# Kernel optimization log

Hardware: AMD Instinct MI355X
Metric: run time of the kernel (lower is better)

Reference implementation:

```python
import jax, jax.numpy as jnp
import numpy as np

N_NODES = 50000
N_EDGES = 800000
IN_CH = 128
OUT_CH = 64
HEADS = 4
NEG_SLOPE = 0.2  # PyG GATConv default


def setup_inputs() -> dict:
    key = jax.random.key(0)
    k1, k2, k3, k4, k5 = jax.random.split(key, 5)
    x = jax.random.normal(k1, (N_NODES, IN_CH), dtype=jnp.float32)
    edge_index = jax.random.randint(k2, (2, N_EDGES), 0, N_NODES, dtype=jnp.int64)
    W = jax.random.normal(k3, (HEADS * OUT_CH, IN_CH), dtype=jnp.float32) * (1.0 / np.sqrt(IN_CH))
    att_src = jax.random.normal(k4, (HEADS, OUT_CH), dtype=jnp.float32) * (1.0 / np.sqrt(OUT_CH))
    att_dst = jax.random.normal(k5, (HEADS, OUT_CH), dtype=jnp.float32) * (1.0 / np.sqrt(OUT_CH))
    bias = jnp.zeros((OUT_CH,), dtype=jnp.float32)
    return {"x": x, "edge_index": edge_index, "W": W,
            "att_src": att_src, "att_dst": att_dst, "bias": bias}


def reference(x, edge_index, W, att_src, att_dst, bias):
    # GAT2NO_NORM.forward in eval mode: dropout == identity.
    N = x.shape[0]
    H, C = att_src.shape
    # PyG GATConv adds self-loops by default.
    loop = jnp.arange(N, dtype=edge_index.dtype)
    src = jnp.concatenate([edge_index[0], loop])  # message source j
    dst = jnp.concatenate([edge_index[1], loop])  # message target i
    # Linear projection, reshape to heads: [N, H, C]
    h = (x @ W.T).reshape(N, H, C)
    # Per-node attention halves: [N, H]
    a_src = jnp.einsum('nhc,hc->nh', h, att_src)
    a_dst = jnp.einsum('nhc,hc->nh', h, att_dst)
    # Per-edge raw score, LeakyReLU: [E, H]
    e = jax.nn.leaky_relu(a_src[src] + a_dst[dst], NEG_SLOPE)
    # Segment (edge-)softmax over incoming edges of each dst node.
    m = jax.lax.stop_gradient(jax.ops.segment_max(e, dst, num_segments=N))
    ex = jnp.exp(e - m[dst])
    denom = jax.ops.segment_sum(ex, dst, num_segments=N)
    alpha = ex / denom[dst]  # self-loops guarantee denom > 0
    # Weighted scatter-sum of messages: [N, H, C]
    msg = h[src] * alpha[:, :, None]
    out = jax.ops.segment_sum(msg, dst, num_segments=N)
    # concat=False -> mean over heads, then bias, then ReLU (module wrapper)
    out = out.mean(axis=1) + bias
    return jax.nn.relu(out)
```

## Files before the change

kernel.cpp:

```cpp
#include <hip/hip_runtime.h>
#include <hip/hip_fp16.h>
#include <math.h>

#define N_NODES 50000
#define N_EDGES 800000
#define IN_CH 128
#define PROJ_CH 256
#define OUT_CH 64
#define HEADS 4
#define NEG_SLOPE 0.2f
#define CAP 80
#define PROJ_BLOCKS 782
#define GRID_BLOCKS 3125

typedef _Float16 f16x8 __attribute__((ext_vector_type(8)));
typedef _Float16 f16x4 __attribute__((ext_vector_type(4)));
typedef __fp16   hf2   __attribute__((ext_vector_type(2)));
typedef float    f32x4 __attribute__((ext_vector_type(4)));

__device__ __forceinline__ float leaky(float v) {
    return v > 0.f ? v : NEG_SLOPE * v;
}

__device__ __forceinline__ hf2 u32_as_h2(unsigned int u) {
    union { unsigned int u; hf2 h; } c; c.u = u; return c.h;
}

__global__ __launch_bounds__(256) void prep_kernel(
    const float* __restrict__ W, _Float16* __restrict__ Wh, int* __restrict__ cnt)
{
    const int t = blockIdx.x * 256 + threadIdx.x;
    if (t < PROJ_CH * IN_CH) Wh[t] = (_Float16)W[t];
    if (t < N_NODES) cnt[t] = 0;
}

__global__ __launch_bounds__(256) void mega_kernel(
    const float* __restrict__ x, const _Float16* __restrict__ Wh,
    const float* __restrict__ att_src, const float* __restrict__ att_dst,
    const int* __restrict__ ei, int* __restrict__ cnt, unsigned short* __restrict__ csr,
    _Float16* __restrict__ h, float* __restrict__ a_src, float* __restrict__ a_dst)
{
    __shared__ _Float16 xs[64 * 136];
    const int tid = threadIdx.x;
    const int bid = blockIdx.x;

    const int e = bid * 256 + tid;
    const int esrc = ei[e];
    const int edst = ei[N_EDGES + e];
    const int pos = atomicAdd(&cnt[edst], 1);

    if (bid >= PROJ_BLOCKS) {
        if (pos < CAP) csr[edst * CAP + pos] = (unsigned short)esrc;
        return;
    }

    const int w    = tid >> 6;
    const int lane = tid & 63;
    const int q    = lane >> 4;
    const int l15  = lane & 15;
    const int nb   = bid * 64;

    float4 xv[8];
#pragma unroll
    for (int r = 0; r < 8; ++r) {
        int v   = r * 256 + tid;
        int row = v >> 5;
        int c4  = v & 31;
        int grow = nb + row;
        if (grow > N_NODES - 1) grow = N_NODES - 1;
        xv[r] = *(const float4*)(x + (size_t)grow * IN_CH + c4 * 4);
    }

    f16x8 B[4][4];
#pragma unroll
    for (int k0i = 0; k0i < 4; ++k0i)
#pragma unroll
        for (int n0i = 0; n0i < 4; ++n0i) {
            const int oc = w * 64 + n0i * 16 + l15;
            B[k0i][n0i] = *(const f16x8*)(Wh + (size_t)oc * IN_CH + k0i * 32 + q * 8);
        }

#pragma unroll
    for (int r = 0; r < 8; ++r) {
        int v   = r * 256 + tid;
        int row = v >> 5;
        int c4  = v & 31;
        f16x4 hv;
        hv[0] = (_Float16)xv[r].x; hv[1] = (_Float16)xv[r].y;
        hv[2] = (_Float16)xv[r].z; hv[3] = (_Float16)xv[r].w;
        *(f16x4*)&xs[row * 136 + c4 * 4] = hv;
    }
    __syncthreads();

    f32x4 acc[4][4];
#pragma unroll
    for (int m0i = 0; m0i < 4; ++m0i)
#pragma unroll
        for (int n0i = 0; n0i < 4; ++n0i)
            acc[m0i][n0i] = (f32x4){0.f, 0.f, 0.f, 0.f};

#pragma unroll
    for (int k0i = 0; k0i < 4; ++k0i) {
        f16x8 A[4];
#pragma unroll
        for (int m0i = 0; m0i < 4; ++m0i)
            A[m0i] = *(const f16x8*)&xs[(m0i * 16 + l15) * 136 + k0i * 32 + q * 8];
#pragma unroll
        for (int n0i = 0; n0i < 4; ++n0i)
#pragma unroll
            for (int m0i = 0; m0i < 4; ++m0i)
                acc[m0i][n0i] = __builtin_amdgcn_mfma_f32_16x16x32_f16(
                    A[m0i], B[k0i][n0i], acc[m0i][n0i], 0, 0, 0);
    }

    float att_s[4], att_d[4];
#pragma unroll
    for (int n0i = 0; n0i < 4; ++n0i) {
        att_s[n0i] = att_src[w * 64 + n0i * 16 + l15];
        att_d[n0i] = att_dst[w * 64 + n0i * 16 + l15];
    }

#pragma unroll
    for (int m0i = 0; m0i < 4; ++m0i) {
        float vs[4], vd[4];
#pragma unroll
        for (int r = 0; r < 4; ++r) {
            float s = 0.f, d = 0.f;
#pragma unroll
            for (int n0i = 0; n0i < 4; ++n0i) {
                s = fmaf(acc[m0i][n0i][r], att_s[n0i], s);
                d = fmaf(acc[m0i][n0i][r], att_d[n0i], d);
            }
            vs[r] = s; vd[r] = d;
        }
#pragma unroll
        for (int off = 1; off < 16; off <<= 1) {
#pragma unroll
            for (int r = 0; r < 4; ++r) {
                vs[r] += __shfl_xor(vs[r], off, 64);
                vd[r] += __shfl_xor(vd[r], off, 64);
            }
        }
#pragma unroll
        for (int r = 0; r < 4; ++r) {
            int node = nb + m0i * 16 + q * 4 + r;
            if (l15 == 0 && node < N_NODES) {
                a_src[node * HEADS + w] = vs[r];
                a_dst[node * HEADS + w] = vd[r];
            }
        }
    }

    unsigned char* lb = (unsigned char*)xs;
    __syncthreads();
#pragma unroll
    for (int p = 0; p < 2; ++p) {
#pragma unroll
        for (int mm = 0; mm < 2; ++mm) {
            const int m0i = 2 * p + mm;
            const int nl0 = mm * 16 + q * 4;
#pragma unroll
            for (int n0i = 0; n0i < 4; ++n0i) {
                const int ch = w * 64 + n0i * 16 + l15;
#pragma unroll
                for (int r = 0; r < 4; ++r)
                    *(_Float16*)(lb + (nl0 + r) * 528 + ch * 2) =
                        (_Float16)acc[m0i][n0i][r];
            }
        }
        __syncthreads();
#pragma unroll
        for (int r = 0; r < 4; ++r) {
            int idx  = r * 256 + tid;
            int nl   = idx >> 5;
            int ck   = idx & 31;
            int node = nb + p * 32 + nl;
            if (node < N_NODES) {
                f16x8 vv = *(const f16x8*)(lb + nl * 528 + ck * 16);
                *(f16x8*)(h + (size_t)node * PROJ_CH + ck * 8) = vv;
            }
        }
        if (p == 0) __syncthreads();
    }

    if (pos < CAP) csr[edst * CAP + pos] = (unsigned short)esrc;
}

__global__ __launch_bounds__(256) void aggregate_kernel(
    const _Float16* __restrict__ h, const float* __restrict__ a_src,
    const float* __restrict__ a_dst, const int* __restrict__ cnt,
    const unsigned short* __restrict__ csr, const float* __restrict__ bias,
    float* __restrict__ out)
{
    const int tid  = threadIdx.x;
    const int wave = tid >> 6;
    const int l    = tid & 63;
    const int i    = blockIdx.x * 4 + wave;

    __shared__ float lw_all[4][(CAP + 1) * 4];
    __shared__ int   lj_all[4][CAP + 4];
    float* lw = lw_all[wave];
    int*   lj = lj_all[wave];

    const int n    = min(cnt[i], CAP);
    const int base = i * CAP;
    const int h4   = l & 3;
    const float adh = a_dst[i * 4 + h4];

    float lsum = 0.f;
    {
        float ws = __expf(leaky(a_src[i * 4 + h4] + adh));
        if (l < 4) { lw[l] = ws; lsum = ws; }
        if (l == 0) lj[0] = i;
    }

    const int erel = l >> 2;
    for (int p0 = 0; p0 < n; p0 += 16) {
        int e = p0 + erel;
        bool valid = e < n;
        int j = valid ? (int)csr[base + e] : 0;
        float w = 0.f;
        if (valid) w = __expf(leaky(a_src[j * 4 + h4] + adh));
        lsum += w;
        lw[(e + 1) * 4 + h4] = w;
        if (h4 == 0) lj[e + 1] = j;
    }
#pragma unroll
    for (int off = 4; off < 64; off <<= 1) lsum += __shfl_xor(lsum, off, 64);

    __syncthreads();

    const int half_ = l >> 5;
    const int jj    = l & 31;
    const int hd    = jj >> 3;
    const int m_total = n + 1;
    const uint4* hv = (const uint4*)h;

    float acc[8];
#pragma unroll
    for (int k = 0; k < 8; ++k) acc[k] = 0.f;

    for (int qq = 0; qq < m_total; qq += 16) {
        const int eb = qq + 8 * half_;
        int ia[8]; float wa[8];
#pragma unroll
        for (int k = 0; k < 8; ++k) {
            int e2 = eb + k;
            bool v = e2 < m_total;
            ia[k] = v ? e2 : 0;
            wa[k] = v ? lw[ia[k] * 4 + hd] : 0.f;
        }
        uint4 d[8];
#pragma unroll
        for (int k = 0; k < 8; ++k)
            d[k] = hv[(size_t)lj[ia[k]] * 32 + jj];

        hf2 wp[4];
#pragma unroll
        for (int pr = 0; pr < 4; ++pr)
            wp[pr] = __builtin_amdgcn_cvt_pkrtz(wa[2 * pr], wa[2 * pr + 1]);

#pragma unroll
        for (int pr = 0; pr < 4; ++pr) {
            const unsigned int* Aa = (const unsigned int*)&d[2 * pr];
            const unsigned int* Ab = (const unsigned int*)&d[2 * pr + 1];
#pragma unroll
            for (int k = 0; k < 4; ++k) {
                unsigned int lo = __builtin_amdgcn_perm(Ab[k], Aa[k], 0x05040100u);
                unsigned int hi = __builtin_amdgcn_perm(Ab[k], Aa[k], 0x07060302u);
                acc[2 * k]     = __builtin_amdgcn_fdot2(u32_as_h2(lo), wp[pr], acc[2 * k], false);
                acc[2 * k + 1] = __builtin_amdgcn_fdot2(u32_as_h2(hi), wp[pr], acc[2 * k + 1], false);
            }
        }
    }

#pragma unroll
    for (int k = 0; k < 8; ++k) acc[k] += __shfl_xor(acc[k], 32, 64);

    float linv = 1.f / __shfl(lsum, hd, 64);
#pragma unroll
    for (int k = 0; k < 8; ++k) {
        float r = acc[k] * linv;
        r += __shfl_xor(r, 8, 64);
        r += __shfl_xor(r, 16, 64);
        acc[k] = r;
    }

    if (l < 8) {
        float* op = out + (size_t)i * OUT_CH + l * 8;
        float4 o0, o1;
        o0.x = fmaxf(0.25f * acc[0] + bias[l * 8 + 0], 0.f);
        o0.y = fmaxf(0.25f * acc[1] + bias[l * 8 + 1], 0.f);
        o0.z = fmaxf(0.25f * acc[2] + bias[l * 8 + 2], 0.f);
        o0.w = fmaxf(0.25f * acc[3] + bias[l * 8 + 3], 0.f);
        o1.x = fmaxf(0.25f * acc[4] + bias[l * 8 + 4], 0.f);
        o1.y = fmaxf(0.25f * acc[5] + bias[l * 8 + 5], 0.f);
        o1.z = fmaxf(0.25f * acc[6] + bias[l * 8 + 6], 0.f);
        o1.w = fmaxf(0.25f * acc[7] + bias[l * 8 + 7], 0.f);
        *(float4*)op = o0;
        *((float4*)op + 1) = o1;
    }
}

extern "C" void kernel_launch(void* const* d_in, const int* in_sizes, int n_in,
                              void* d_out, int out_size, void* d_ws, size_t ws_size,
                              hipStream_t stream)
{
    const float* x       = (const float*)d_in[0];
    const int*   ei      = (const int*)d_in[1];
    const float* W       = (const float*)d_in[2];
    const float* att_src = (const float*)d_in[3];
    const float* att_dst = (const float*)d_in[4];
    const float* bias    = (const float*)d_in[5];
    float* out = (float*)d_out;

    _Float16* h   = (_Float16*)d_ws;
    float* asrc  = (float*)(h + (size_t)N_NODES * PROJ_CH);
    float* adst  = asrc + (size_t)N_NODES * HEADS;
    int*   cnt   = (int*)(adst + (size_t)N_NODES * HEADS);
    unsigned short* csr = (unsigned short*)(cnt + N_NODES);
    _Float16* Wh = (_Float16*)(csr + (size_t)N_NODES * CAP);

    hipLaunchKernelGGL(prep_kernel, dim3(196), dim3(256), 0, stream, W, Wh, cnt);
    hipLaunchKernelGGL(mega_kernel, dim3(GRID_BLOCKS), dim3(256), 0, stream,
                       x, Wh, att_src, att_dst, ei, cnt, csr, h, asrc, adst);
    hipLaunchKernelGGL(aggregate_kernel, dim3(N_NODES / 4), dim3(256), 0, stream,
                       h, asrc, adst, cnt, csr, bias, out);
}
```

Baseline: 205.6 us.

## Replicate per-node edge counters and CSR buckets eightfold to spread atomics

Edge binning now uses eight replicated count/CSR buffers chosen by block index, each capped at 20 slots, to cut same-address atomic contention. The aggregate kernel merges the eight buckets into shared memory before computing weights. The projection kernel also moves the atomic after the x load and writes h directly from registers instead of staging through LDS. The trade-off is more counter memory, a larger prep clear, scattered 2-byte h stores, and truncation risk if one replica bucket overflows even when the total degree is small.

```diff
diff --git a/kernel.cpp b/kernel.cpp
--- a/kernel.cpp
+++ b/kernel.cpp
@@ -9,7 +9,9 @@
 #define OUT_CH 64
 #define HEADS 4
 #define NEG_SLOPE 0.2f
-#define CAP 80
+#define NREP 8
+#define CAP8 20
+#define CAPT (NREP * CAP8)
 #define PROJ_BLOCKS 782
 #define GRID_BLOCKS 3125
 
@@ -27,30 +29,31 @@
 }
 
 __global__ __launch_bounds__(256) void prep_kernel(
-    const float* __restrict__ W, _Float16* __restrict__ Wh, int* __restrict__ cnt)
+    const float* __restrict__ W, _Float16* __restrict__ Wh, int* __restrict__ cnt8)
 {
     const int t = blockIdx.x * 256 + threadIdx.x;
     if (t < PROJ_CH * IN_CH) Wh[t] = (_Float16)W[t];
-    if (t < N_NODES) cnt[t] = 0;
+    if (t < NREP * N_NODES) cnt8[t] = 0;
 }
 
 __global__ __launch_bounds__(256) void mega_kernel(
     const float* __restrict__ x, const _Float16* __restrict__ Wh,
     const float* __restrict__ att_src, const float* __restrict__ att_dst,
-    const int* __restrict__ ei, int* __restrict__ cnt, unsigned short* __restrict__ csr,
+    const int* __restrict__ ei, int* __restrict__ cnt8, unsigned short* __restrict__ csr8,
     _Float16* __restrict__ h, float* __restrict__ a_src, float* __restrict__ a_dst)
 {
     __shared__ _Float16 xs[64 * 136];
     const int tid = threadIdx.x;
     const int bid = blockIdx.x;
+    const int rep = bid & (NREP - 1);
 
     const int e = bid * 256 + tid;
     const int esrc = ei[e];
     const int edst = ei[N_EDGES + e];
-    const int pos = atomicAdd(&cnt[edst], 1);
 
     if (bid >= PROJ_BLOCKS) {
-        if (pos < CAP) csr[edst * CAP + pos] = (unsigned short)esrc;
+        int pos = atomicAdd(&cnt8[rep * N_NODES + edst], 1);
+        if (pos < CAP8) csr8[((size_t)rep * N_NODES + edst) * CAP8 + pos] = (unsigned short)esrc;
         return;
     }
 
@@ -60,7 +63,15 @@
     const int l15  = lane & 15;
     const int nb   = bid * 64;
 
-    float4 xv[8];
+    f16x8 B[4][4];
+#pragma unroll
+    for (int k0i = 0; k0i < 4; ++k0i)
+#pragma unroll
+        for (int n0i = 0; n0i < 4; ++n0i) {
+            const int oc = w * 64 + n0i * 16 + l15;
+            B[k0i][n0i] = *(const f16x8*)(Wh + (size_t)oc * IN_CH + k0i * 32 + q * 8);
+        }
+
 #pragma unroll
     for (int r = 0; r < 8; ++r) {
         int v   = r * 256 + tid;
@@ -68,29 +79,15 @@
         int c4  = v & 31;
         int grow = nb + row;
         if (grow > N_NODES - 1) grow = N_NODES - 1;
-        xv[r] = *(const float4*)(x + (size_t)grow * IN_CH + c4 * 4);
-    }
-
-    f16x8 B[4][4];
-#pragma unroll
-    for (int k0i = 0; k0i < 4; ++k0i)
-#pragma unroll
-        for (int n0i = 0; n0i < 4; ++n0i) {
-            const int oc = w * 64 + n0i * 16 + l15;
-            B[k0i][n0i] = *(const f16x8*)(Wh + (size_t)oc * IN_CH + k0i * 32 + q * 8);
-        }
-
-#pragma unroll
-    for (int r = 0; r < 8; ++r) {
-        int v   = r * 256 + tid;
-        int row = v >> 5;
-        int c4  = v & 31;
+        float4 xv = *(const float4*)(x + (size_t)grow * IN_CH + c4 * 4);
         f16x4 hv;
-        hv[0] = (_Float16)xv[r].x; hv[1] = (_Float16)xv[r].y;
-        hv[2] = (_Float16)xv[r].z; hv[3] = (_Float16)xv[r].w;
+        hv[0] = (_Float16)xv.x; hv[1] = (_Float16)xv.y;
+        hv[2] = (_Float16)xv.z; hv[3] = (_Float16)xv.w;
         *(f16x4*)&xs[row * 136 + c4 * 4] = hv;
     }
     __syncthreads();
+
+    const int pos = atomicAdd(&cnt8[rep * N_NODES + edst], 1);
 
     f32x4 acc[4][4];
 #pragma unroll
@@ -149,47 +146,25 @@
                 a_dst[node * HEADS + w] = vd[r];
             }
         }
-    }
-
-    unsigned char* lb = (unsigned char*)xs;
-    __syncthreads();
-#pragma unroll
-    for (int p = 0; p < 2; ++p) {
-#pragma unroll
-        for (int mm = 0; mm < 2; ++mm) {
-            const int m0i = 2 * p + mm;
-            const int nl0 = mm * 16 + q * 4;
-#pragma unroll
-            for (int n0i = 0; n0i < 4; ++n0i) {
-                const int ch = w * 64 + n0i * 16 + l15;
-#pragma unroll
-                for (int r = 0; r < 4; ++r)
-                    *(_Float16*)(lb + (nl0 + r) * 528 + ch * 2) =
+#pragma unroll
+        for (int r = 0; r < 4; ++r) {
+            int node = nb + m0i * 16 + q * 4 + r;
+            if (node < N_NODES) {
+#pragma unroll
+                for (int n0i = 0; n0i < 4; ++n0i)
+                    h[(size_t)node * PROJ_CH + w * 64 + n0i * 16 + l15] =
                         (_Float16)acc[m0i][n0i][r];
             }
         }
-        __syncthreads();
-#pragma unroll
-        for (int r = 0; r < 4; ++r) {
-            int idx  = r * 256 + tid;
-            int nl   = idx >> 5;
-            int ck   = idx & 31;
-            int node = nb + p * 32 + nl;
-            if (node < N_NODES) {
-                f16x8 vv = *(const f16x8*)(lb + nl * 528 + ck * 16);
-                *(f16x8*)(h + (size_t)node * PROJ_CH + ck * 8) = vv;
-            }
-        }
-        if (p == 0) __syncthreads();
-    }
-
-    if (pos < CAP) csr[edst * CAP + pos] = (unsigned short)esrc;
+    }
+
+    if (pos < CAP8) csr8[((size_t)rep * N_NODES + edst) * CAP8 + pos] = (unsigned short)esrc;
 }
 
 __global__ __launch_bounds__(256) void aggregate_kernel(
     const _Float16* __restrict__ h, const float* __restrict__ a_src,
-    const float* __restrict__ a_dst, const int* __restrict__ cnt,
-    const unsigned short* __restrict__ csr, const float* __restrict__ bias,
+    const float* __restrict__ a_dst, const int* __restrict__ cnt8,
+    const unsigned short* __restrict__ csr8, const float* __restrict__ bias,
     float* __restrict__ out)
 {
     const int tid  = threadIdx.x;
@@ -197,13 +172,31 @@
     const int l    = tid & 63;
     const int i    = blockIdx.x * 4 + wave;
 
-    __shared__ float lw_all[4][(CAP + 1) * 4];
-    __shared__ int   lj_all[4][CAP + 4];
+    __shared__ float lw_all[4][(CAPT + 1) * 4];
+    __shared__ int   lj_all[4][CAPT + 4];
     float* lw = lw_all[wave];
     int*   lj = lj_all[wave];
 
-    const int n    = min(cnt[i], CAP);
-    const int base = i * CAP;
+    const int gr = l >> 3;
+    const int gk = l & 7;
+    int nr_g = 0, base_g = 0, m = 0;
+#pragma unroll
+    for (int r = 0; r < NREP; ++r) {
+        int c = cnt8[r * N_NODES + i];
+        c = min(c, CAP8);
+        if (r == gr) { nr_g = c; base_g = m; }
+        m += c;
+    }
+    if (l == 0) lj[0] = i;
+    {
+        const size_t cbase = ((size_t)gr * N_NODES + i) * CAP8;
+#pragma unroll
+        for (int kk = 0; kk < CAP8; kk += 8) {
+            int k = gk + kk;
+            if (k < nr_g) lj[1 + base_g + k] = (int)csr8[cbase + k];
+        }
+    }
+
     const int h4   = l & 3;
     const float adh = a_dst[i * 4 + h4];
 
@@ -211,19 +204,17 @@
     {
         float ws = __expf(leaky(a_src[i * 4 + h4] + adh));
         if (l < 4) { lw[l] = ws; lsum = ws; }
-        if (l == 0) lj[0] = i;
     }
 
     const int erel = l >> 2;
-    for (int p0 = 0; p0 < n; p0 += 16) {
+    for (int p0 = 0; p0 < m; p0 += 16) {
         int e = p0 + erel;
-        bool valid = e < n;
-        int j = valid ? (int)csr[base + e] : 0;
+        bool valid = e < m;
+        int j = valid ? lj[e + 1] : 0;
         float w = 0.f;
         if (valid) w = __expf(leaky(a_src[j * 4 + h4] + adh));
         lsum += w;
         lw[(e + 1) * 4 + h4] = w;
-        if (h4 == 0) lj[e + 1] = j;
     }
 #pragma unroll
     for (int off = 4; off < 64; off <<= 1) lsum += __shfl_xor(lsum, off, 64);
@@ -233,7 +224,7 @@
     const int half_ = l >> 5;
     const int jj    = l & 31;
     const int hd    = jj >> 3;
-    const int m_total = n + 1;
+    const int m_total = m + 1;
     const uint4* hv = (const uint4*)h;
 
     float acc[8];
@@ -314,16 +305,17 @@
     const float* bias    = (const float*)d_in[5];
     float* out = (float*)d_out;
 
-    _Float16* h   = (_Float16*)d_ws;
+    _Float16* h  = (_Float16*)d_ws;
     float* asrc  = (float*)(h + (size_t)N_NODES * PROJ_CH);
     float* adst  = asrc + (size_t)N_NODES * HEADS;
-    int*   cnt   = (int*)(adst + (size_t)N_NODES * HEADS);
-    unsigned short* csr = (unsigned short*)(cnt + N_NODES);
-    _Float16* Wh = (_Float16*)(csr + (size_t)N_NODES * CAP);
-
-    hipLaunchKernelGGL(prep_kernel, dim3(196), dim3(256), 0, stream, W, Wh, cnt);
+    int*   cnt8  = (int*)(adst + (size_t)N_NODES * HEADS);
+    unsigned short* csr8 = (unsigned short*)(cnt8 + NREP * N_NODES);
+    _Float16* Wh = (_Float16*)(csr8 + (size_t)NREP * N_NODES * CAP8);
+
+    hipLaunchKernelGGL(prep_kernel, dim3((NREP * N_NODES + 255) / 256), dim3(256), 0, stream,
+                       W, Wh, cnt8);
     hipLaunchKernelGGL(mega_kernel, dim3(GRID_BLOCKS), dim3(256), 0, stream,
-                       x, Wh, att_src, att_dst, ei, cnt, csr, h, asrc, adst);
+                       x, Wh, att_src, att_dst, ei, cnt8, csr8, h, asrc, adst);
     hipLaunchKernelGGL(aggregate_kernel, dim3(N_NODES / 4), dim3(256), 0, stream,
-                       h, asrc, adst, cnt, csr, bias, out);
-}
+                       h, asrc, adst, cnt8, csr8, bias, out);
+}
```

Result: no change. 202.8 us (-1.4%).
